# Kernel optimization log

Hardware: AMD Instinct MI355X
Metric: run time of the kernel (lower is better)

Reference implementation:

```python
import jax, jax.numpy as jnp
import numpy as np

B, T, F = 8192, 30, 16
H1, H2 = 64, 32


def _lstm(x, Wih, Whh, b):
    """PyTorch-convention LSTM (gate order i,f,g,o). x: [B,T,I] -> (ys [B,T,H], hT [B,H])."""
    H = Whh.shape[1]
    h0 = jnp.zeros((x.shape[0], H), x.dtype)

    def step(carry, xt):
        h, c = carry
        z = xt @ Wih.T + h @ Whh.T + b  # [B,4H]
        i, f, g, o = jnp.split(z, 4, axis=-1)
        c = jax.nn.sigmoid(f) * c + jax.nn.sigmoid(i) * jnp.tanh(g)
        h = jax.nn.sigmoid(o) * jnp.tanh(c)
        return (h, c), h

    (hT, _), ys = jax.lax.scan(step, (h0, h0), jnp.swapaxes(x, 0, 1))
    return jnp.swapaxes(ys, 0, 1), hT


def setup_inputs() -> dict:
    key = jax.random.key(0)
    ks = jax.random.split(key, 16)
    s = 0.1  # small init scale for numerical sanity
    return {
        "x": jax.random.normal(ks[0], (B, T, F), jnp.float32),
        "Wih1": jax.random.normal(ks[1], (4 * H1, F), jnp.float32) * s,
        "Whh1": jax.random.normal(ks[2], (4 * H1, H1), jnp.float32) * s,
        "b1": jax.random.normal(ks[3], (4 * H1,), jnp.float32) * s,
        "Wih2": jax.random.normal(ks[4], (4 * H2, H1), jnp.float32) * s,
        "Whh2": jax.random.normal(ks[5], (4 * H2, H2), jnp.float32) * s,
        "b2": jax.random.normal(ks[6], (4 * H2,), jnp.float32) * s,
        "Wih3": jax.random.normal(ks[7], (4 * H2, H2), jnp.float32) * s,
        "Whh3": jax.random.normal(ks[8], (4 * H2, H2), jnp.float32) * s,
        "b3": jax.random.normal(ks[9], (4 * H2,), jnp.float32) * s,
        "Wih4": jax.random.normal(ks[10], (4 * H1, H2), jnp.float32) * s,
        "Whh4": jax.random.normal(ks[11], (4 * H1, H1), jnp.float32) * s,
        "b4": jax.random.normal(ks[12], (4 * H1,), jnp.float32) * s,
        "Wout": jax.random.normal(ks[13], (F, H1), jnp.float32) * s,
        "bout": jax.random.normal(ks[14], (F,), jnp.float32) * s,
    }


def reference(x, Wih1, Whh1, b1, Wih2, Whh2, b2, Wih3, Whh3, b3, Wih4, Whh4, b4, Wout, bout):
    ys1, _ = _lstm(x, Wih1, Whh1, b1)          # encoder LSTM(64)
    _, latent = _lstm(ys1, Wih2, Whh2, b2)      # encoder LSTM(32) -> final hidden [B,32]
    repeated = jnp.broadcast_to(latent[:, None, :], (latent.shape[0], T, latent.shape[1]))
    ys3, _ = _lstm(repeated, Wih3, Whh3, b3)    # decoder LSTM(32)
    ys4, _ = _lstm(ys3, Wih4, Whh4, b4)         # decoder LSTM(64)
    return ys4 @ Wout.T + bout                  # [B,T,F]
```

## Files before the change

kernel.cpp:

```cpp
#include <hip/hip_runtime.h>


#define TT 30
#define FF 16
#define NT 768

typedef unsigned short u16t;
typedef __attribute__((ext_vector_type(8))) short short8;
typedef __attribute__((ext_vector_type(4))) short short4v;
typedef __attribute__((ext_vector_type(4))) float floatx4;

#define MFMA(a, b, c) __builtin_amdgcn_mfma_f32_16x16x32_bf16(a, b, c, 0, 0, 0)

#if __has_builtin(__builtin_amdgcn_exp2f)
#define EXP2(x) __builtin_amdgcn_exp2f(x)
#else
#define EXP2(x) exp2f(x)
#endif

template <int P> struct IC { static constexpr int v = P; };

__device__ __forceinline__ float rcpf(float v) { return __builtin_amdgcn_rcpf(v); }
__device__ __forceinline__ u16t f2bf(float f) {
  unsigned int u = __float_as_uint(f);
  u = (u + 0x7FFFu + ((u >> 16) & 1u)) >> 16;
  return (u16t)u;
}
__device__ __forceinline__ short8 ldFragS(const float* p, float s) {
  const float4 lo = *(const float4*)p;
  const float4 hi = *(const float4*)(p + 4);
  short8 r;
  r[0] = (short)f2bf(lo.x * s); r[1] = (short)f2bf(lo.y * s);
  r[2] = (short)f2bf(lo.z * s); r[3] = (short)f2bf(lo.w * s);
  r[4] = (short)f2bf(hi.x * s); r[5] = (short)f2bf(hi.y * s);
  r[6] = (short)f2bf(hi.z * s); r[7] = (short)f2bf(hi.w * s);
  return r;
}
__device__ __forceinline__ float cellUp(const floatx4 acc, float& c) {
  float ei = EXP2(-acc[0]);
  float ef = EXP2(-acc[1]);
  float eg = EXP2(-acc[2]);
  float eo = EXP2(-acc[3]);
  float fv = rcpf(1.f + ef);
  float P  = (1.f - eg) * rcpf((1.f + ei) * (1.f + eg));
  c = fv * c + P;
  float ec = EXP2(-2.885390082f * c);
  return (1.f - ec) * rcpf((1.f + eo) * (1.f + ec));
}

__global__ __launch_bounds__(NT, 6) void lstm_ae_mfma7(
    const float* __restrict__ x,
    const float* __restrict__ Wih1, const float* __restrict__ Whh1, const float* __restrict__ b1,
    const float* __restrict__ Wih2, const float* __restrict__ Whh2, const float* __restrict__ b2,
    const float* __restrict__ Wih3, const float* __restrict__ Whh3, const float* __restrict__ b3,
    const float* __restrict__ Wih4, const float* __restrict__ Whh4, const float* __restrict__ b4,
    const float* __restrict__ Wout, const float* __restrict__ bout,
    float* __restrict__ out)
{
  __shared__ __align__(16) u16t xAll[16 * 968];
  __shared__ __align__(16) u16t aB[16 * 264];

  const int t = threadIdx.x;
  const int w = t >> 6, lane = t & 63;
  const int q = lane >> 4, n = lane & 15;
  const int q8 = q * 8, n264 = n * 264, n968 = n * 968;
  const int bBase = blockIdx.x * 16;
  const int nlo = n >> 2, ngt = n & 3;
  const u16t* aRow = &aB[n264];
  const bool isZ1 = (w < 8);
  const int u = w & 3;

  const float L1 = 1.442695041f, L2 = 2.885390082f;
  const float sA = (ngt == 2) ? L2 : L1;

  for (int i = t; i < 16 * 264; i += NT) aB[i] = 0;
  {
    const float* xb = x + (size_t)bBase * (TT * FF);
    for (int i4 = t; i4 < 1920; i4 += NT) {
      int e = i4 * 4;
      int b = e / 480, r = e - b * 480;
      int stp = r >> 4, f = r & 15;
      float4 v = *(const float4*)&xb[e];
      short4v s4 = { (short)f2bf(v.x), (short)f2bf(v.y), (short)f2bf(v.z), (short)f2bf(v.w) };
      *(short4v*)&xAll[b * 968 + stp * 32 + f] = s4;
    }
    for (int i = t; i < 7680; i += NT) {
      int b = i / 480, r = i - b * 480;
      int stp = r >> 4, f = r & 15;
      xAll[b * 968 + stp * 32 + 16 + f] = 0;
    }
  }
  const short8 z8 = { 0, 0, 0, 0, 0, 0, 0, 0 };
  short8 wAf[2][3]; floatx4 biasA[2];
  if (isZ1) {
#pragma unroll
    for (int tt = 0; tt < 2; ++tt) {
      int T = w + 8 * tt;
      int row = ngt * 64 + T * 4 + nlo;
      wAf[tt][0] = z8;
      if (q < 2) wAf[tt][0] = ldFragS(&Wih1[row * 16 + q8], sA);
      wAf[tt][1] = ldFragS(&Whh1[row * 64 + q8], sA);
      wAf[tt][2] = ldFragS(&Whh1[row * 64 + 32 + q8], sA);
#pragma unroll
      for (int r = 0; r < 4; ++r) biasA[tt][r] = b1[r * 64 + T * 4 + q] * (r == 2 ? L2 : L1);
    }
  } else {
#pragma unroll
    for (int tt = 0; tt < 2; ++tt) {
      int T = 2 * u + tt;
      int row = ngt * 32 + T * 4 + nlo;
      wAf[tt][0] = ldFragS(&Wih2[row * 64 + q8], sA);
      wAf[tt][1] = ldFragS(&Wih2[row * 64 + 32 + q8], sA);
      wAf[tt][2] = ldFragS(&Whh2[row * 32 + q8], sA);
#pragma unroll
      for (int r = 0; r < 4; ++r) biasA[tt][r] = b2[r * 32 + T * 4 + q] * (r == 2 ? L2 : L1);
    }
  }
  if (blockIdx.x & 256) {
    __builtin_amdgcn_s_sleep(15);
    __builtin_amdgcn_s_sleep(15);
  }
  __syncthreads();

  float cA[2] = {0.f, 0.f};
  short8 bxN;

  if (isZ1) {
    const short8 bx = *(const short8*)&xAll[n968 + q8];
#pragma unroll
    for (int tt = 0; tt < 2; ++tt) {
      floatx4 a0 = biasA[tt];
      a0 = MFMA(wAf[tt][0], bx, a0);
      aB[n264 + (w + 8 * tt) * 4 + q] = f2bf(cellUp(a0, cA[tt]));
    }
    bxN = *(const short8*)&xAll[n968 + 32 + q8];
  }
  __syncthreads();

  auto stepA = [&](int st, auto pc) {
    constexpr int p = decltype(pc)::v;
    const short8 bh1a = *(const short8*)&aRow[p * 64 + q8];
    const short8 bh1b = *(const short8*)&aRow[p * 64 + 32 + q8];
    if (isZ1) {
#pragma unroll
      for (int tt = 0; tt < 2; ++tt) {
        floatx4 a0 = biasA[tt];
        a0 = MFMA(wAf[tt][0], bxN, a0);
        a0 = MFMA(wAf[tt][1], bh1a, a0);
        a0 = MFMA(wAf[tt][2], bh1b, a0);
        aB[n264 + (1 - p) * 64 + (w + 8 * tt) * 4 + q] = f2bf(cellUp(a0, cA[tt]));
      }
      const int nx = (st + 2 < TT) ? st + 2 : TT - 1;
      bxN = *(const short8*)&xAll[n968 + nx * 32 + q8];
    } else {
      const short8 bh2 = *(const short8*)&aRow[128 + (1 - p) * 32 + q8];
#pragma unroll
      for (int tt = 0; tt < 2; ++tt) {
        floatx4 a2 = biasA[tt];
        a2 = MFMA(wAf[tt][0], bh1a, a2);
        a2 = MFMA(wAf[tt][1], bh1b, a2);
        a2 = MFMA(wAf[tt][2], bh2, a2);
        aB[n264 + 128 + p * 32 + (2 * u + tt) * 4 + q] = f2bf(cellUp(a2, cA[tt]));
      }
    }
    __syncthreads();
  };
  for (int st = 0; st < 28; st += 2) { stepA(st, IC<0>{}); stepA(st + 1, IC<1>{}); }
  stepA(28, IC<0>{});
  if (!isZ1) {
    const short8 bh1a = *(const short8*)&aRow[64 + q8];
    const short8 bh1b = *(const short8*)&aRow[96 + q8];
    const short8 bh2  = *(const short8*)&aRow[128 + q8];
#pragma unroll
    for (int tt = 0; tt < 2; ++tt) {
      floatx4 a2 = biasA[tt];
      a2 = MFMA(wAf[tt][0], bh1a, a2);
      a2 = MFMA(wAf[tt][1], bh1b, a2);
      a2 = MFMA(wAf[tt][2], bh2, a2);
      aB[n264 + 160 + (2 * u + tt) * 4 + q] = f2bf(cellUp(a2, cA[tt]));
    }
  }
  __syncthreads();

  short8 wBf[2][3]; floatx4 biasB[2];
  short8 wof[2]; floatx4 biasO;
  short8 blat;
  if (isZ1) {
#pragma unroll
    for (int tt = 0; tt < 2; ++tt) {
      int T = w + 8 * tt;
      int row = ngt * 64 + T * 4 + nlo;
      wBf[tt][0] = ldFragS(&Wih4[row * 32 + q8], sA);
      wBf[tt][1] = ldFragS(&Whh4[row * 64 + q8], sA);
      wBf[tt][2] = ldFragS(&Whh4[row * 64 + 32 + q8], sA);
#pragma unroll
      for (int r = 0; r < 4; ++r) biasB[tt][r] = b4[r * 64 + T * 4 + q] * (r == 2 ? L2 : L1);
    }
    wof[0] = ldFragS(&Wout[n * 64 + q8], 1.f);
    wof[1] = ldFragS(&Wout[n * 64 + 32 + q8], 1.f);
    biasO = *(const floatx4*)&bout[q * 4];
  } else {
#pragma unroll
    for (int tt = 0; tt < 2; ++tt) {
      int T = 2 * u + tt;
      int row = ngt * 32 + T * 4 + nlo;
      wBf[tt][0] = ldFragS(&Wih3[row * 32 + q8], sA);
      wBf[tt][1] = ldFragS(&Whh3[row * 32 + q8], sA);
#pragma unroll
      for (int r = 0; r < 4; ++r) biasB[tt][r] = b3[r * 32 + T * 4 + q] * (r == 2 ? L2 : L1);
    }
    blat = *(const short8*)&aRow[160 + q8];
  }
  for (int i = t; i < 1024; i += NT) aB[(i >> 6) * 264 + 64 + (i & 63)] = 0;
  __syncthreads();

  float cB[2] = {0.f, 0.f};

  if (!isZ1) {
#pragma unroll
    for (int tt = 0; tt < 2; ++tt) {
      floatx4 a3 = biasB[tt];
      a3 = MFMA(wBf[tt][0], blat, a3);
      aB[n264 + 192 + (2 * u + tt) * 4 + q] = f2bf(cellUp(a3, cB[tt]));
    }
  }
  __syncthreads();

  auto stepB = [&](int st, auto pc) {
    constexpr int p = decltype(pc)::v;
    const short8 bh3 = *(const short8*)&aRow[192 + p * 32 + q8];
    if (isZ1) {
      const short8 bh4a = *(const short8*)&aRow[(1 - p) * 64 + q8];
      const short8 bh4b = *(const short8*)&aRow[(1 - p) * 64 + 32 + q8];
#pragma unroll
      for (int tt = 0; tt < 2; ++tt) {
        floatx4 a4 = biasB[tt];
        a4 = MFMA(wBf[tt][0], bh3, a4);
        a4 = MFMA(wBf[tt][1], bh4a, a4);
        a4 = MFMA(wBf[tt][2], bh4b, a4);
        aB[n264 + p * 64 + (w + 8 * tt) * 4 + q] = f2bf(cellUp(a4, cB[tt]));
      }
      if (st > 0 && w == ((st - 1) & 7)) {
        floatx4 yv = biasO;
        yv = MFMA(wof[0], bh4a, yv);
        yv = MFMA(wof[1], bh4b, yv);
        *(floatx4*)&out[((size_t)(bBase + n) * TT + (st - 1)) * FF + q * 4] = yv;
      }
    } else {
#pragma unroll
      for (int tt = 0; tt < 2; ++tt) {
        floatx4 a3 = biasB[tt];
        a3 = MFMA(wBf[tt][0], blat, a3);
        a3 = MFMA(wBf[tt][1], bh3, a3);
        aB[n264 + 192 + (1 - p) * 32 + (2 * u + tt) * 4 + q] = f2bf(cellUp(a3, cB[tt]));
      }
    }
    __syncthreads();
  };
  for (int st = 0; st < 28; st += 2) { stepB(st, IC<0>{}); stepB(st + 1, IC<1>{}); }
  stepB(28, IC<0>{});
  if (isZ1) {
    const short8 bh3  = *(const short8*)&aRow[224 + q8];
    const short8 bh4a = *(const short8*)&aRow[q8];
    const short8 bh4b = *(const short8*)&aRow[32 + q8];
#pragma unroll
    for (int tt = 0; tt < 2; ++tt) {
      floatx4 a4 = biasB[tt];
      a4 = MFMA(wBf[tt][0], bh3, a4);
      a4 = MFMA(wBf[tt][1], bh4a, a4);
      a4 = MFMA(wBf[tt][2], bh4b, a4);
      aB[n264 + 64 + (w + 8 * tt) * 4 + q] = f2bf(cellUp(a4, cB[tt]));
    }
    if (w == 4) {
      floatx4 yv = biasO;
      yv = MFMA(wof[0], bh4a, yv);
      yv = MFMA(wof[1], bh4b, yv);
      *(floatx4*)&out[((size_t)(bBase + n) * TT + 28) * FF + q * 4] = yv;
    }
  }
  __syncthreads();
  if (w == 5) {
    const short8 ba = *(const short8*)&aRow[64 + q8];
    const short8 bb = *(const short8*)&aRow[96 + q8];
    floatx4 yv = biasO;
    yv = MFMA(wof[0], ba, yv);
    yv = MFMA(wof[1], bb, yv);
    *(floatx4*)&out[((size_t)(bBase + n) * TT + 29) * FF + q * 4] = yv;
  }
}

extern "C" void kernel_launch(void* const* d_in, const int* in_sizes, int n_in,
                              void* d_out, int out_size, void* d_ws, size_t ws_size,
                              hipStream_t stream) {
  const float* x    = (const float*)d_in[0];
  const float* Wih1 = (const float*)d_in[1];
  const float* Whh1 = (const float*)d_in[2];
  const float* b1   = (const float*)d_in[3];
  const float* Wih2 = (const float*)d_in[4];
  const float* Whh2 = (const float*)d_in[5];
  const float* b2   = (const float*)d_in[6];
  const float* Wih3 = (const float*)d_in[7];
  const float* Whh3 = (const float*)d_in[8];
  const float* b3   = (const float*)d_in[9];
  const float* Wih4 = (const float*)d_in[10];
  const float* Whh4 = (const float*)d_in[11];
  const float* b4   = (const float*)d_in[12];
  const float* Wout = (const float*)d_in[13];
  const float* bout = (const float*)d_in[14];
  float* out = (float*)d_out;

  const int B = in_sizes[0] / (TT * FF);
  dim3 grid(B / 16), block(NT);
  lstm_ae_mfma7<<<grid, block, 0, stream>>>(
      x, Wih1, Whh1, b1, Wih2, Whh2, b2, Wih3, Whh3, b3,
      Wih4, Whh4, b4, Wout, bout, out);
}
```

Baseline: 165.7 us.

## Process 32 batch rows per block with two interleaved MFMA chains

Each block now handles 32 batch rows instead of 16. Every wave runs two independent MFMA accumulation chains and cell updates per step, reusing the same register-resident weight fragments. This halves the grid and the number of per-step barriers per batch row, and gives each wave more independent work to hide MFMA and transcendental latency. In exchange it doubles LDS per block, lowers the launch-bounds occupancy target from 6 to 3, and removes the s_sleep staggering of half the blocks, so fewer blocks are resident at once.

```diff
diff --git a/kernel.cpp b/kernel.cpp
--- a/kernel.cpp
+++ b/kernel.cpp
@@ -48,7 +48,7 @@
   return (1.f - ec) * rcpf((1.f + eo) * (1.f + ec));
 }
 
-__global__ __launch_bounds__(NT, 6) void lstm_ae_mfma7(
+__global__ __launch_bounds__(NT, 3) void lstm_ae_mfma8(
     const float* __restrict__ x,
     const float* __restrict__ Wih1, const float* __restrict__ Whh1, const float* __restrict__ b1,
     const float* __restrict__ Wih2, const float* __restrict__ Whh2, const float* __restrict__ b2,
@@ -57,26 +57,27 @@
     const float* __restrict__ Wout, const float* __restrict__ bout,
     float* __restrict__ out)
 {
-  __shared__ __align__(16) u16t xAll[16 * 968];
-  __shared__ __align__(16) u16t aB[16 * 264];
+  __shared__ __align__(16) u16t xAll[32 * 968];
+  __shared__ __align__(16) u16t aB[32 * 264];
 
   const int t = threadIdx.x;
   const int w = t >> 6, lane = t & 63;
   const int q = lane >> 4, n = lane & 15;
-  const int q8 = q * 8, n264 = n * 264, n968 = n * 968;
-  const int bBase = blockIdx.x * 16;
+  const int q8 = q * 8;
+  const int bBase = blockIdx.x * 32;
   const int nlo = n >> 2, ngt = n & 3;
-  const u16t* aRow = &aB[n264];
+  const int r0 = n * 264, r1 = (n + 16) * 264;
+  const int x0 = n * 968, x1 = (n + 16) * 968;
   const bool isZ1 = (w < 8);
   const int u = w & 3;
 
   const float L1 = 1.442695041f, L2 = 2.885390082f;
   const float sA = (ngt == 2) ? L2 : L1;
 
-  for (int i = t; i < 16 * 264; i += NT) aB[i] = 0;
+  for (int i = t; i < 32 * 264; i += NT) aB[i] = 0;
   {
     const float* xb = x + (size_t)bBase * (TT * FF);
-    for (int i4 = t; i4 < 1920; i4 += NT) {
+    for (int i4 = t; i4 < 3840; i4 += NT) {
       int e = i4 * 4;
       int b = e / 480, r = e - b * 480;
       int stp = r >> 4, f = r & 15;
@@ -84,7 +85,7 @@
       short4v s4 = { (short)f2bf(v.x), (short)f2bf(v.y), (short)f2bf(v.z), (short)f2bf(v.w) };
       *(short4v*)&xAll[b * 968 + stp * 32 + f] = s4;
     }
-    for (int i = t; i < 7680; i += NT) {
+    for (int i = t; i < 15360; i += NT) {
       int b = i / 480, r = i - b * 480;
       int stp = r >> 4, f = r & 15;
       xAll[b * 968 + stp * 32 + 16 + f] = 0;
@@ -116,51 +117,63 @@
       for (int r = 0; r < 4; ++r) biasA[tt][r] = b2[r * 32 + T * 4 + q] * (r == 2 ? L2 : L1);
     }
   }
-  if (blockIdx.x & 256) {
-    __builtin_amdgcn_s_sleep(15);
-    __builtin_amdgcn_s_sleep(15);
-  }
-  __syncthreads();
-
-  float cA[2] = {0.f, 0.f};
-  short8 bxN;
+  __syncthreads();
+
+  float cA[2][2] = {{0.f, 0.f}, {0.f, 0.f}};
+  short8 bxN[2];
 
   if (isZ1) {
-    const short8 bx = *(const short8*)&xAll[n968 + q8];
-#pragma unroll
-    for (int tt = 0; tt < 2; ++tt) {
-      floatx4 a0 = biasA[tt];
-      a0 = MFMA(wAf[tt][0], bx, a0);
-      aB[n264 + (w + 8 * tt) * 4 + q] = f2bf(cellUp(a0, cA[tt]));
-    }
-    bxN = *(const short8*)&xAll[n968 + 32 + q8];
+    const short8 bx0 = *(const short8*)&xAll[x0 + q8];
+    const short8 bx1 = *(const short8*)&xAll[x1 + q8];
+#pragma unroll
+    for (int tt = 0; tt < 2; ++tt) {
+      floatx4 a0 = biasA[tt], a1 = biasA[tt];
+      a0 = MFMA(wAf[tt][0], bx0, a0);
+      a1 = MFMA(wAf[tt][0], bx1, a1);
+      aB[r0 + (w + 8 * tt) * 4 + q] = f2bf(cellUp(a0, cA[0][tt]));
+      aB[r1 + (w + 8 * tt) * 4 + q] = f2bf(cellUp(a1, cA[1][tt]));
+    }
+    bxN[0] = *(const short8*)&xAll[x0 + 32 + q8];
+    bxN[1] = *(const short8*)&xAll[x1 + 32 + q8];
   }
   __syncthreads();
 
   auto stepA = [&](int st, auto pc) {
     constexpr int p = decltype(pc)::v;
-    const short8 bh1a = *(const short8*)&aRow[p * 64 + q8];
-    const short8 bh1b = *(const short8*)&aRow[p * 64 + 32 + q8];
+    const short8 h1a0 = *(const short8*)&aB[r0 + p * 64 + q8];
+    const short8 h1b0 = *(const short8*)&aB[r0 + p * 64 + 32 + q8];
+    const short8 h1a1 = *(const short8*)&aB[r1 + p * 64 + q8];
+    const short8 h1b1 = *(const short8*)&aB[r1 + p * 64 + 32 + q8];
     if (isZ1) {
 #pragma unroll
       for (int tt = 0; tt < 2; ++tt) {
-        floatx4 a0 = biasA[tt];
-        a0 = MFMA(wAf[tt][0], bxN, a0);
-        a0 = MFMA(wAf[tt][1], bh1a, a0);
-        a0 = MFMA(wAf[tt][2], bh1b, a0);
-        aB[n264 + (1 - p) * 64 + (w + 8 * tt) * 4 + q] = f2bf(cellUp(a0, cA[tt]));
+        floatx4 a0 = biasA[tt], a1 = biasA[tt];
+        a0 = MFMA(wAf[tt][0], bxN[0], a0);
+        a1 = MFMA(wAf[tt][0], bxN[1], a1);
+        a0 = MFMA(wAf[tt][1], h1a0, a0);
+        a1 = MFMA(wAf[tt][1], h1a1, a1);
+        a0 = MFMA(wAf[tt][2], h1b0, a0);
+        a1 = MFMA(wAf[tt][2], h1b1, a1);
+        aB[r0 + (1 - p) * 64 + (w + 8 * tt) * 4 + q] = f2bf(cellUp(a0, cA[0][tt]));
+        aB[r1 + (1 - p) * 64 + (w + 8 * tt) * 4 + q] = f2bf(cellUp(a1, cA[1][tt]));
       }
       const int nx = (st + 2 < TT) ? st + 2 : TT - 1;
-      bxN = *(const short8*)&xAll[n968 + nx * 32 + q8];
+      bxN[0] = *(const short8*)&xAll[x0 + nx * 32 + q8];
+      bxN[1] = *(const short8*)&xAll[x1 + nx * 32 + q8];
     } else {
-      const short8 bh2 = *(const short8*)&aRow[128 + (1 - p) * 32 + q8];
+      const short8 h20 = *(const short8*)&aB[r0 + 128 + (1 - p) * 32 + q8];
+      const short8 h21 = *(const short8*)&aB[r1 + 128 + (1 - p) * 32 + q8];
 #pragma unroll
       for (int tt = 0; tt < 2; ++tt) {
-        floatx4 a2 = biasA[tt];
-        a2 = MFMA(wAf[tt][0], bh1a, a2);
-        a2 = MFMA(wAf[tt][1], bh1b, a2);
-        a2 = MFMA(wAf[tt][2], bh2, a2);
-        aB[n264 + 128 + p * 32 + (2 * u + tt) * 4 + q] = f2bf(cellUp(a2, cA[tt]));
+        floatx4 a0 = biasA[tt], a1 = biasA[tt];
+        a0 = MFMA(wAf[tt][0], h1a0, a0);
+        a1 = MFMA(wAf[tt][0], h1a1, a1);
+        a0 = MFMA(wAf[tt][1], h1b0, a0);
+        a1 = MFMA(wAf[tt][1], h1b1, a1);
+        a0 = MFMA(wAf[tt][2], h20, a0);
+        a1 = MFMA(wAf[tt][2], h21, a1);
+        aB[r0 + 128 + p * 32 + (2 * u + tt) * 4 + q] = f2bf(cellUp(a0, cA[0][tt]));
+        aB[r1 + 128 + p * 32 + (2 * u + tt) * 4 + q] = f2bf(cellUp(a1, cA[1][tt]));
       }
     }
     __syncthreads();
@@ -168,23 +181,30 @@
   for (int st = 0; st < 28; st += 2) { stepA(st, IC<0>{}); stepA(st + 1, IC<1>{}); }
   stepA(28, IC<0>{});
   if (!isZ1) {
-    const short8 bh1a = *(const short8*)&aRow[64 + q8];
-    const short8 bh1b = *(const short8*)&aRow[96 + q8];
-    const short8 bh2  = *(const short8*)&aRow[128 + q8];
-#pragma unroll
-    for (int tt = 0; tt < 2; ++tt) {
-      floatx4 a2 = biasA[tt];
-      a2 = MFMA(wAf[tt][0], bh1a, a2);
-      a2 = MFMA(wAf[tt][1], bh1b, a2);
-      a2 = MFMA(wAf[tt][2], bh2, a2);
-      aB[n264 + 160 + (2 * u + tt) * 4 + q] = f2bf(cellUp(a2, cA[tt]));
+    const short8 h1a0 = *(const short8*)&aB[r0 + 64 + q8];
+    const short8 h1b0 = *(const short8*)&aB[r0 + 96 + q8];
+    const short8 h1a1 = *(const short8*)&aB[r1 + 64 + q8];
+    const short8 h1b1 = *(const short8*)&aB[r1 + 96 + q8];
+    const short8 h20  = *(const short8*)&aB[r0 + 128 + q8];
+    const short8 h21  = *(const short8*)&aB[r1 + 128 + q8];
+#pragma unroll
+    for (int tt = 0; tt < 2; ++tt) {
+      floatx4 a0 = biasA[tt], a1 = biasA[tt];
+      a0 = MFMA(wAf[tt][0], h1a0, a0);
+      a1 = MFMA(wAf[tt][0], h1a1, a1);
+      a0 = MFMA(wAf[tt][1], h1b0, a0);
+      a1 = MFMA(wAf[tt][1], h1b1, a1);
+      a0 = MFMA(wAf[tt][2], h20, a0);
+      a1 = MFMA(wAf[tt][2], h21, a1);
+      aB[r0 + 160 + (2 * u + tt) * 4 + q] = f2bf(cellUp(a0, cA[0][tt]));
+      aB[r1 + 160 + (2 * u + tt) * 4 + q] = f2bf(cellUp(a1, cA[1][tt]));
     }
   }
   __syncthreads();
 
   short8 wBf[2][3]; floatx4 biasB[2];
   short8 wof[2]; floatx4 biasO;
-  short8 blat;
+  short8 blat[2];
   if (isZ1) {
 #pragma unroll
     for (int tt = 0; tt < 2; ++tt) {
@@ -209,50 +229,66 @@
 #pragma unroll
       for (int r = 0; r < 4; ++r) biasB[tt][r] = b3[r * 32 + T * 4 + q] * (r == 2 ? L2 : L1);
     }
-    blat = *(const short8*)&aRow[160 + q8];
-  }
-  for (int i = t; i < 1024; i += NT) aB[(i >> 6) * 264 + 64 + (i & 63)] = 0;
-  __syncthreads();
-
-  float cB[2] = {0.f, 0.f};
+    blat[0] = *(const short8*)&aB[r0 + 160 + q8];
+    blat[1] = *(const short8*)&aB[r1 + 160 + q8];
+  }
+  for (int i = t; i < 2048; i += NT) aB[(i >> 6) * 264 + 64 + (i & 63)] = 0;
+  __syncthreads();
+
+  float cB[2][2] = {{0.f, 0.f}, {0.f, 0.f}};
 
   if (!isZ1) {
 #pragma unroll
     for (int tt = 0; tt < 2; ++tt) {
-      floatx4 a3 = biasB[tt];
-      a3 = MFMA(wBf[tt][0], blat, a3);
-      aB[n264 + 192 + (2 * u + tt) * 4 + q] = f2bf(cellUp(a3, cB[tt]));
+      floatx4 a0 = biasB[tt], a1 = biasB[tt];
+      a0 = MFMA(wBf[tt][0], blat[0], a0);
+      a1 = MFMA(wBf[tt][0], blat[1], a1);
+      aB[r0 + 192 + (2 * u + tt) * 4 + q] = f2bf(cellUp(a0, cB[0][tt]));
+      aB[r1 + 192 + (2 * u + tt) * 4 + q] = f2bf(cellUp(a1, cB[1][tt]));
     }
   }
   __syncthreads();
 
   auto stepB = [&](int st, auto pc) {
     constexpr int p = decltype(pc)::v;
-    const short8 bh3 = *(const short8*)&aRow[192 + p * 32 + q8];
+    const short8 h30 = *(const short8*)&aB[r0 + 192 + p * 32 + q8];
+    const short8 h31 = *(const short8*)&aB[r1 + 192 + p * 32 + q8];
     if (isZ1) {
-      const short8 bh4a = *(const short8*)&aRow[(1 - p) * 64 + q8];
-      const short8 bh4b = *(const short8*)&aRow[(1 - p) * 64 + 32 + q8];
+      const short8 h4a0 = *(const short8*)&aB[r0 + (1 - p) * 64 + q8];
+      const short8 h4b0 = *(const short8*)&aB[r0 + (1 - p) * 64 + 32 + q8];
+      const short8 h4a1 = *(const short8*)&aB[r1 + (1 - p) * 64 + q8];
+      const short8 h4b1 = *(const short8*)&aB[r1 + (1 - p) * 64 + 32 + q8];
 #pragma unroll
       for (int tt = 0; tt < 2; ++tt) {
-        floatx4 a4 = biasB[tt];
-        a4 = MFMA(wBf[tt][0], bh3, a4);
-        a4 = MFMA(wBf[tt][1], bh4a, a4);
-        a4 = MFMA(wBf[tt][2], bh4b, a4);
-        aB[n264 + p * 64 + (w + 8 * tt) * 4 + q] = f2bf(cellUp(a4, cB[tt]));
+        floatx4 a0 = biasB[tt], a1 = biasB[tt];
+        a0 = MFMA(wBf[tt][0], h30, a0);
+        a1 = MFMA(wBf[tt][0], h31, a1);
+        a0 = MFMA(wBf[tt][1], h4a0, a0);
+        a1 = MFMA(wBf[tt][1], h4a1, a1);
+        a0 = MFMA(wBf[tt][2], h4b0, a0);
+        a1 = MFMA(wBf[tt][2], h4b1, a1);
+        aB[r0 + p * 64 + (w + 8 * tt) * 4 + q] = f2bf(cellUp(a0, cB[0][tt]));
+        aB[r1 + p * 64 + (w + 8 * tt) * 4 + q] = f2bf(cellUp(a1, cB[1][tt]));
       }
       if (st > 0 && w == ((st - 1) & 7)) {
-        floatx4 yv = biasO;
-        yv = MFMA(wof[0], bh4a, yv);
-        yv = MFMA(wof[1], bh4b, yv);
-        *(floatx4*)&out[((size_t)(bBase + n) * TT + (st - 1)) * FF + q * 4] = yv;
+        floatx4 y0 = biasO, y1 = biasO;
+        y0 = MFMA(wof[0], h4a0, y0);
+        y1 = MFMA(wof[0], h4a1, y1);
+        y0 = MFMA(wof[1], h4b0, y0);
+        y1 = MFMA(wof[1], h4b1, y1);
+        *(floatx4*)&out[((size_t)(bBase + n) * TT + (st - 1)) * FF + q * 4] = y0;
+        *(floatx4*)&out[((size_t)(bBase + n + 16) * TT + (st - 1)) * FF + q * 4] = y1;
       }
     } else {
 #pragma unroll
       for (int tt = 0; tt < 2; ++tt) {
-        floatx4 a3 = biasB[tt];
-        a3 = MFMA(wBf[tt][0], blat, a3);
-        a3 = MFMA(wBf[tt][1], bh3, a3);
-        aB[n264 + 192 + (1 - p) * 32 + (2 * u + tt) * 4 + q] = f2bf(cellUp(a3, cB[tt]));
+        floatx4 a0 = biasB[tt], a1 = biasB[tt];
+        a0 = MFMA(wBf[tt][0], blat[0], a0);
+        a1 = MFMA(wBf[tt][0], blat[1], a1);
+        a0 = MFMA(wBf[tt][1], h30, a0);
+        a1 = MFMA(wBf[tt][1], h31, a1);
+        aB[r0 + 192 + (1 - p) * 32 + (2 * u + tt) * 4 + q] = f2bf(cellUp(a0, cB[0][tt]));
+        aB[r1 + 192 + (1 - p) * 32 + (2 * u + tt) * 4 + q] = f2bf(cellUp(a1, cB[1][tt]));
       }
     }
     __syncthreads();
@@ -260,32 +296,47 @@
   for (int st = 0; st < 28; st += 2) { stepB(st, IC<0>{}); stepB(st + 1, IC<1>{}); }
   stepB(28, IC<0>{});
   if (isZ1) {
-    const short8 bh3  = *(const short8*)&aRow[224 + q8];
-    const short8 bh4a = *(const short8*)&aRow[q8];
-    const short8 bh4b = *(const short8*)&aRow[32 + q8];
-#pragma unroll
-    for (int tt = 0; tt < 2; ++tt) {
-      floatx4 a4 = biasB[tt];
-      a4 = MFMA(wBf[tt][0], bh3, a4);
-      a4 = MFMA(wBf[tt][1], bh4a, a4);
-      a4 = MFMA(wBf[tt][2], bh4b, a4);
-      aB[n264 + 64 + (w + 8 * tt) * 4 + q] = f2bf(cellUp(a4, cB[tt]));
+    const short8 h30  = *(const short8*)&aB[r0 + 224 + q8];
+    const short8 h31  = *(const short8*)&aB[r1 + 224 + q8];
+    const short8 h4a0 = *(const short8*)&aB[r0 + q8];
+    const short8 h4b0 = *(const short8*)&aB[r0 + 32 + q8];
+    const short8 h4a1 = *(const short8*)&aB[r1 + q8];
+    const short8 h4b1 = *(const short8*)&aB[r1 + 32 + q8];
+#pragma unroll
+    for (int tt = 0; tt < 2; ++tt) {
+      floatx4 a0 = biasB[tt], a1 = biasB[tt];
+      a0 = MFMA(wBf[tt][0], h30, a0);
+      a1 = MFMA(wBf[tt][0], h31, a1);
+      a0 = MFMA(wBf[tt][1], h4a0, a0);
+      a1 = MFMA(wBf[tt][1], h4a1, a1);
+      a0 = MFMA(wBf[tt][2], h4b0, a0);
+      a1 = MFMA(wBf[tt][2], h4b1, a1);
+      aB[r0 + 64 + (w + 8 * tt) * 4 + q] = f2bf(cellUp(a0, cB[0][tt]));
+      aB[r1 + 64 + (w + 8 * tt) * 4 + q] = f2bf(cellUp(a1, cB[1][tt]));
     }
     if (w == 4) {
-      floatx4 yv = biasO;
-      yv = MFMA(wof[0], bh4a, yv);
-      yv = MFMA(wof[1], bh4b, yv);
-      *(floatx4*)&out[((size_t)(bBase + n) * TT + 28) * FF + q * 4] = yv;
+      floatx4 y0 = biasO, y1 = biasO;
+      y0 = MFMA(wof[0], h4a0, y0);
+      y1 = MFMA(wof[0], h4a1, y1);
+      y0 = MFMA(wof[1], h4b0, y0);
+      y1 = MFMA(wof[1], h4b1, y1);
+      *(floatx4*)&out[((size_t)(bBase + n) * TT + 28) * FF + q * 4] = y0;
+      *(floatx4*)&out[((size_t)(bBase + n + 16) * TT + 28) * FF + q * 4] = y1;
     }
   }
   __syncthreads();
   if (w == 5) {
-    const short8 ba = *(const short8*)&aRow[64 + q8];
-    const short8 bb = *(const short8*)&aRow[96 + q8];
-    floatx4 yv = biasO;
-    yv = MFMA(wof[0], ba, yv);
-    yv = MFMA(wof[1], bb, yv);
-    *(floatx4*)&out[((size_t)(bBase + n) * TT + 29) * FF + q * 4] = yv;
+    const short8 ba0 = *(const short8*)&aB[r0 + 64 + q8];
+    const short8 bb0 = *(const short8*)&aB[r0 + 96 + q8];
+    const short8 ba1 = *(const short8*)&aB[r1 + 64 + q8];
+    const short8 bb1 = *(const short8*)&aB[r1 + 96 + q8];
+    floatx4 y0 = biasO, y1 = biasO;
+    y0 = MFMA(wof[0], ba0, y0);
+    y1 = MFMA(wof[0], ba1, y1);
+    y0 = MFMA(wof[1], bb0, y0);
+    y1 = MFMA(wof[1], bb1, y1);
+    *(floatx4*)&out[((size_t)(bBase + n) * TT + 29) * FF + q * 4] = y0;
+    *(floatx4*)&out[((size_t)(bBase + n + 16) * TT + 29) * FF + q * 4] = y1;
   }
 }
 
@@ -310,8 +361,8 @@
   float* out = (float*)d_out;
 
   const int B = in_sizes[0] / (TT * FF);
-  dim3 grid(B / 16), block(NT);
-  lstm_ae_mfma7<<<grid, block, 0, stream>>>(
+  dim3 grid(B / 32), block(NT);
+  lstm_ae_mfma8<<<grid, block, 0, stream>>>(
       x, Wih1, Whh1, b1, Wih2, Whh2, b2, Wih3, Whh3, b3,
       Wih4, Whh4, b4, Wout, bout, out);
 }
```

New measurement: 158.9 us. 4.1% less time.
